# Kernel optimization log

Hardware: AMD Instinct MI355X
Metric: run time of the kernel (lower is better)

The kernel has to match this reference:

```python
import jax, jax.numpy as jnp
import numpy as np

H, QP, VP, D, DP = 4, 4, 4, 128, 64
DH = D // H


def setup_inputs() -> dict:
    key = jax.random.key(0)
    ks = jax.random.split(key, 16)
    B, L = 1, 1024
    w_c0 = float(np.log(np.e - 1.0))
    inp = {
        'single': jax.random.normal(ks[0], (B, L, D), jnp.float32),
        'pair': jax.random.normal(ks[1], (B, L, L, DP), jnp.float32),
        'T': jax.random.normal(ks[2], (B, L, 4, 4), jnp.float32),
        'w_C': jnp.full((H,), w_c0, jnp.float32),
        'ln_g': jnp.ones((D,), jnp.float32),
        'ln_b': jnp.zeros((D,), jnp.float32),
        'Wq': jax.random.normal(ks[3], (D, H * DH), jnp.float32) * 0.05,
        'Wk': jax.random.normal(ks[4], (D, H * DH), jnp.float32) * 0.05,
        'Wv': jax.random.normal(ks[5], (D, H * DH), jnp.float32) * 0.05,
        'Wqpt': jax.random.normal(ks[6], (D, H * QP * 3), jnp.float32) * 0.05,
        'Wkpt': jax.random.normal(ks[7], (D, H * QP * 3), jnp.float32) * 0.05,
        'Wvpt': jax.random.normal(ks[8], (D, H * VP * 3), jnp.float32) * 0.05,
        'Wb': jax.random.normal(ks[9], (DP, H), jnp.float32) * 0.05,
        'Wout': jax.random.normal(ks[10], (H * (DH + DP + VP * 3 + VP), D), jnp.float32) * 0.05,
        'b_out': jnp.zeros((D,), jnp.float32),
    }
    return inp


def _layernorm(x, g, b, eps=1e-5):
    x32 = x.astype(jnp.float32)
    mu = x32.mean(-1, keepdims=True)
    var = ((x32 - mu) ** 2).mean(-1, keepdims=True)
    return ((x32 - mu) * jax.lax.rsqrt(var + eps) * g + b).astype(x.dtype)


def reference(single, pair, T, w_C, ln_g, ln_b, Wq, Wk, Wv, Wqpt, Wkpt, Wvpt, Wb, Wout, b_out):
    B, L, Dm = single.shape
    scale_attn = DH ** (-0.5)
    z = _layernorm(single, ln_g, ln_b)
    Q = (z @ Wq).reshape(B, L, H, DH)
    K = (z @ Wk).reshape(B, L, H, DH)
    V = (z @ Wv).reshape(B, L, H, DH)
    Q_pt = (z @ Wqpt).reshape(B, L, H, QP, 3)
    K_pt = (z @ Wkpt).reshape(B, L, H, QP, 3)
    V_pt = (z @ Wvpt).reshape(B, L, H, VP, 3)
    R = T[..., :3, :3]   # [B,L,3,3]
    t = T[..., :3, 3]    # [B,L,3]
    # global-frame points: R @ p + t
    Q_g = jnp.einsum('blxy,blhpy->blhpx', R, Q_pt) + t[:, :, None, None, :]
    K_g = jnp.einsum('blxy,blhpy->blhpx', R, K_pt) + t[:, :, None, None, :]
    V_g = jnp.einsum('blxy,blhpy->blhpx', R, V_pt) + t[:, :, None, None, :]
    # scalar QK score [B,H,L,L]
    s_attn = jnp.einsum('bihd,bjhd->bhij', Q, K) * scale_attn
    # pair bias [B,H,L,L]
    b_attn = jnp.einsum('bijc,ch->bhij', pair, Wb)
    # squared point distance [B,H,L,L]
    diff = Q_g[:, :, None] - K_g[:, None]          # [B,L,L,H,QP,3]
    d2 = jnp.moveaxis((diff ** 2).sum((-1, -2)), -1, 1)
    w_pt = jax.nn.softplus(w_C)[None, :, None, None]
    attn = jax.nn.softmax(s_attn + b_attn - 0.5 * w_pt * d2, axis=-1)
    # scalar values [B,L,H*DH]
    o_s = jnp.einsum('bhij,bjhd->bihd', attn, V).reshape(B, L, H * DH)
    # point values aggregated in global frame then mapped back: R^T (p - t)
    o_pt_g = jnp.einsum('bhij,bjhpx->bihpx', attn, V_g)
    o_pt = jnp.einsum('blyx,blhpy->blhpx', R, o_pt_g - t[:, :, None, None, :])
    o_pt_n = jnp.sqrt((o_pt ** 2).sum(-1))
    # pair aggregation [B,L,H*DP]
    o_pair = jnp.einsum('bhij,bijc->bihc', attn, pair).reshape(B, L, H * DP)
    out = jnp.concatenate([o_s, o_pair, o_pt.reshape(B, L, -1), o_pt_n.reshape(B, L, -1)], axis=-1)
    return single + out @ Wout + b_out
```

## Files before the change

### kernel.cpp

```cpp
#include <hip/hip_runtime.h>
#include <math.h>

#define L_SEQ 1024
#define DM 128
#define JC 32
#define NCH (L_SEQ / JC)

#define OFF_KHAT 0
#define OFF_QHAT (L_SEQ * 192)
#define OFF_V    (OFF_QHAT + L_SEQ * 192)
#define OFF_VG   (OFF_V + L_SEQ * DM)

typedef __attribute__((address_space(1))) const void* gas_t;
typedef __attribute__((address_space(3))) void* las_t;

__device__ __forceinline__ void async16(const float4* g, float4* l) {
    __builtin_amdgcn_global_load_lds((gas_t)g, (las_t)l, 16, 0, 0);
}
#define ASYNC_BAR() asm volatile("s_waitcnt lgkmcnt(0)\n\ts_barrier" ::: "memory")

__global__ __launch_bounds__(256) void ipa_prep(
    const float* __restrict__ single, const float* __restrict__ T,
    const float* __restrict__ w_C, const float* __restrict__ ln_g, const float* __restrict__ ln_b,
    const float* __restrict__ Wq, const float* __restrict__ Wk, const float* __restrict__ Wv,
    const float* __restrict__ Wqpt, const float* __restrict__ Wkpt, const float* __restrict__ Wvpt,
    float* __restrict__ ws)
{
    __shared__ float z_lds[4][128];
    __shared__ float proj[4][528];
    __shared__ float qg[4][4][4][3];
    __shared__ float kg[4][4][4][3];
    __shared__ float cq[4][4], ck[4][4];

    const int t = threadIdx.x;
    const int wv = t >> 6, lane = t & 63;
    const int i0 = blockIdx.x << 2;
    const int i = i0 + wv;

    float x0 = single[i*DM + lane];
    float x1 = single[i*DM + 64 + lane];
    float s = x0 + x1, s2 = x0*x0 + x1*x1;
    #pragma unroll
    for (int off = 1; off < 64; off <<= 1) { s += __shfl_xor(s, off); s2 += __shfl_xor(s2, off); }
    float mu = s * 0.0078125f;
    float var = s2 * 0.0078125f - mu*mu;
    float rs = rsqrtf(var + 1e-5f);
    z_lds[wv][lane]      = (x0 - mu) * rs * ln_g[lane]      + ln_b[lane];
    z_lds[wv][lane + 64] = (x1 - mu) * rs * ln_g[lane + 64] + ln_b[lane + 64];
    __syncthreads();

    for (int cc = t; cc < 528; cc += 256) {
        const float* W; int col, ncol;
        if (cc < 128)      { W = Wq;   col = cc;       ncol = 128; }
        else if (cc < 256) { W = Wk;   col = cc - 128; ncol = 128; }
        else if (cc < 384) { W = Wv;   col = cc - 256; ncol = 128; }
        else if (cc < 432) { W = Wqpt; col = cc - 384; ncol = 48;  }
        else if (cc < 480) { W = Wkpt; col = cc - 432; ncol = 48;  }
        else               { W = Wvpt; col = cc - 480; ncol = 48;  }
        float a0 = 0.f, a1 = 0.f, a2 = 0.f, a3 = 0.f;
        #pragma unroll 8
        for (int k = 0; k < 128; ++k) {
            float w = W[k*ncol + col];
            a0 = fmaf(z_lds[0][k], w, a0);
            a1 = fmaf(z_lds[1][k], w, a1);
            a2 = fmaf(z_lds[2][k], w, a2);
            a3 = fmaf(z_lds[3][k], w, a3);
        }
        proj[0][cc] = a0; proj[1][cc] = a1; proj[2][cc] = a2; proj[3][cc] = a3;
    }
    __syncthreads();

    if (t < 64) {
        int r = t >> 4, h = (t >> 2) & 3, p = t & 3;
        int ii = i0 + r;
        float R[3][3], tt[3];
        #pragma unroll
        for (int x = 0; x < 3; ++x) {
            #pragma unroll
            for (int y = 0; y < 3; ++y) R[x][y] = T[ii*16 + x*4 + y];
            tt[x] = T[ii*16 + x*4 + 3];
        }
        int base = 384 + (h*4 + p)*3;
        float q0 = proj[r][base],    q1 = proj[r][base+1],  q2 = proj[r][base+2];
        float k0 = proj[r][base+48], k1 = proj[r][base+49], k2 = proj[r][base+50];
        float v0 = proj[r][base+96], v1 = proj[r][base+97], v2 = proj[r][base+98];
        #pragma unroll
        for (int x = 0; x < 3; ++x) {
            float qq = R[x][0]*q0 + R[x][1]*q1 + R[x][2]*q2 + tt[x];
            float kk = R[x][0]*k0 + R[x][1]*k1 + R[x][2]*k2 + tt[x];
            float vv = R[x][0]*v0 + R[x][1]*v1 + R[x][2]*v2 + tt[x];
            qg[r][h][p][x] = qq;
            kg[r][h][p][x] = kk;
            ws[OFF_VG + ii*48 + h*12 + p*3 + x] = vv;
        }
    }
    __syncthreads();

    if (t < 32) {
        int r = t >> 3, h = (t >> 1) & 3, isk = t & 1;
        float w = w_C[h];
        float wp = log1pf(__expf(w));
        float sq = 0.f;
        #pragma unroll
        for (int p = 0; p < 4; ++p)
            #pragma unroll
            for (int x = 0; x < 3; ++x) {
                float g = isk ? kg[r][h][p][x] : qg[r][h][p][x];
                sq += g*g;
            }
        float c = -0.5f * wp * sq;
        if (isk) ck[r][h] = c; else cq[r][h] = c;
    }
    __syncthreads();

    for (int idx = t; idx < 512; idx += 256) {
        int r = idx >> 7, d = idx & 127;
        ws[OFF_V + (size_t)(i0 + r)*DM + d] = proj[r][256 + d];
    }
    const float scale_attn = 0.17677669529663687f;
    for (int idx = t; idx < 768; idx += 256) {
        int r = idx / 192, rem = idx % 192;
        int h = rem / 48, k = rem % 48;
        int ii = i0 + r;
        float w = w_C[h];
        float wp = log1pf(__expf(w));
        float kv, qv;
        if (k < 32) {
            kv = proj[r][128 + h*32 + k];
            qv = scale_attn * proj[r][h*32 + k];
        } else if (k < 44) {
            int e = k - 32;
            kv = kg[r][h][e/3][e%3];
            qv = wp * qg[r][h][e/3][e%3];
        } else if (k == 44) { kv = ck[r][h]; qv = 1.0f; }
        else if (k == 45)   { kv = 1.0f;    qv = cq[r][h]; }
        else                { kv = 0.f;     qv = 0.f; }
        ws[OFF_KHAT + (size_t)ii*192 + h*48 + k] = kv;
        ws[OFF_QHAT + (size_t)ii*192 + h*48 + k] = qv;
    }
}

__global__ __launch_bounds__(256, 2) void ipa_attn(
    const float* __restrict__ single, const float* __restrict__ pair,
    const float* __restrict__ T, const float* __restrict__ Wb,
    const float* __restrict__ Wout, const float* __restrict__ b_out,
    const float* __restrict__ ws, float* __restrict__ out)
{
    __shared__ __align__(16) float4 pair_lds[2][2][JC][16];
    __shared__ float bias_part[4][2][JC][5];
    __shared__ float p_lds[4][2][JC];
    __shared__ float alpha_lds[4][2];
    __shared__ float l_lds[4][2];
    __shared__ __align__(16) float4 qhat_lds[2][4][12];
    __shared__ __align__(16) float4 wb_lds[64];
    __shared__ float og_lds[2][4][12];
    __shared__ __align__(16) float u_lds[2][448];

    const int t = threadIdx.x;
    const int wv = t >> 6, lane = t & 63;
    const int i0 = blockIdx.x * 2;

    if (t < 96)       ((float4*)qhat_lds)[t] = ((const float4*)(ws + OFF_QHAT))[(size_t)i0*48 + t];
    else if (t < 160) wb_lds[t - 96] = ((const float4*)Wb)[t - 96];

    const int r_b = lane >> 5, j_b = lane & 31;
    const int r_s = lane & 1,  j_s = lane >> 1;
    const int d4  = lane & 7,  jg_s = lane >> 3;
    const int c4p = lane >> 4, jg_p = lane & 15;
    const int g4  = lane & 3,  jg_g = lane >> 2;
    const int g4c = (g4 < 3) ? g4 : 0;

    float m_run = -INFINITY, l_run = 0.f;
    float4 accp[2][4];
    float4 accs[2];
    float4 accg[2];
    #pragma unroll
    for (int r = 0; r < 2; ++r) {
        accs[r] = make_float4(0.f,0.f,0.f,0.f);
        accg[r] = make_float4(0.f,0.f,0.f,0.f);
        #pragma unroll
        for (int h = 0; h < 4; ++h) accp[r][h] = make_float4(0.f,0.f,0.f,0.f);
    }

    const float4* pair4 = (const float4*)pair;
    const float4* kh4   = (const float4*)(ws + OFF_KHAT);
    const float4* v4    = (const float4*)(ws + OFF_V);
    const float4* vg4   = (const float4*)(ws + OFF_VG);
    float4* plds_flat   = &pair_lds[0][0][0][0];

    {
        #pragma unroll
        for (int it = 0; it < 4; ++it) {
            int idx = it*256 + t;
            int row = idx >> 9, j = (idx >> 4) & 31, slot = idx & 15;
            int c4 = slot ^ (j & 7);
            async16(pair4 + ((size_t)(i0 + row)*L_SEQ + j)*16 + c4, plds_flat + idx);
        }
    }

    for (int ch = 0; ch < NCH; ++ch) {
        const int cur = ch & 1;
        const int j0 = ch * JC;

        ASYNC_BAR();
        if (ch + 1 < NCH) {
            const int jn = (ch + 1) * JC;
            #pragma unroll
            for (int it = 0; it < 4; ++it) {
                int idx = it*256 + t;
                int row = idx >> 9, j = (idx >> 4) & 31, slot = idx & 15;
                int c4 = slot ^ (j & 7);
                async16(pair4 + ((size_t)(i0 + row)*L_SEQ + jn + j)*16 + c4,
                        plds_flat + (1 - cur)*1024 + idx);
            }
            asm volatile("s_waitcnt vmcnt(4)" ::: "memory");
        } else {
            asm volatile("s_waitcnt vmcnt(0)" ::: "memory");
        }
        ASYNC_BAR();

        float4 kh[12];
        {
            const float4* kp = kh4 + (size_t)(j0 + j_s)*48 + wv*12;
            #pragma unroll
            for (int k4 = 0; k4 < 12; ++k4) kh[k4] = kp[k4];
        }
        float4 vv[4];
        #pragma unroll
        for (int jj = 0; jj < 4; ++jj)
            vv[jj] = v4[(size_t)(j0 + jg_s + 8*jj)*32 + wv*8 + d4];
        float4 gvv[2];
        #pragma unroll
        for (int jj = 0; jj < 2; ++jj)
            gvv[jj] = vg4[(size_t)(j0 + jg_g + 16*jj)*12 + wv*3 + g4c];

        {
            float bx=0.f, by=0.f, bz=0.f, bw=0.f;
            #pragma unroll
            for (int cp = 0; cp < 4; ++cp) {
                int c4 = (wv << 2) + cp;
                int sw = c4 ^ (j_b & 7);
                float4 pv = pair_lds[cur][r_b][j_b][sw];
                float4 w0 = wb_lds[c4*4+0], w1 = wb_lds[c4*4+1], w2 = wb_lds[c4*4+2], w3 = wb_lds[c4*4+3];
                bx += pv.x*w0.x + pv.y*w1.x + pv.z*w2.x + pv.w*w3.x;
                by += pv.x*w0.y + pv.y*w1.y + pv.z*w2.y + pv.w*w3.y;
                bz += pv.x*w0.z + pv.y*w1.z + pv.z*w2.z + pv.w*w3.z;
                bw += pv.x*w0.w + pv.y*w1.w + pv.z*w2.w + pv.w*w3.w;
            }
            bias_part[wv][r_b][j_b][0] = bx; bias_part[wv][r_b][j_b][1] = by;
            bias_part[wv][r_b][j_b][2] = bz; bias_part[wv][r_b][j_b][3] = bw;
        }
        ASYNC_BAR();

        {
            float d = 0.f;
            #pragma unroll
            for (int k4 = 0; k4 < 12; ++k4) {
                float4 q = qhat_lds[r_s][wv][k4];
                d = fmaf(kh[k4].x, q.x, d); d = fmaf(kh[k4].y, q.y, d);
                d = fmaf(kh[k4].z, q.z, d); d = fmaf(kh[k4].w, q.w, d);
            }
            float bias = bias_part[0][r_s][j_s][wv] + bias_part[1][r_s][j_s][wv]
                       + bias_part[2][r_s][j_s][wv] + bias_part[3][r_s][j_s][wv];
            float logit = d + bias;
            float cmax = logit;
            #pragma unroll
            for (int off = 2; off < 64; off <<= 1) cmax = fmaxf(cmax, __shfl_xor(cmax, off));
            float mn = fmaxf(m_run, cmax);
            float alpha = __expf(m_run - mn);
            float p = __expf(logit - mn);
            float ps = p;
            #pragma unroll
            for (int off = 2; off < 64; off <<= 1) ps += __shfl_xor(ps, off);
            l_run = l_run * alpha + ps;
            m_run = mn;
            p_lds[wv][r_s][j_s] = p;
            if (j_s == 0) alpha_lds[wv][r_s] = alpha;
        }
        ASYNC_BAR();

        {
            float al[4][2];
            #pragma unroll
            for (int h = 0; h < 4; ++h) { al[h][0] = alpha_lds[h][0]; al[h][1] = alpha_lds[h][1]; }
            #pragma unroll
            for (int r = 0; r < 2; ++r) {
                #pragma unroll
                for (int h = 0; h < 4; ++h) {
                    float a = al[h][r];
                    accp[r][h].x *= a; accp[r][h].y *= a; accp[r][h].z *= a; accp[r][h].w *= a;
                }
                float a = al[wv][r];
                accs[r].x *= a; accs[r].y *= a; accs[r].z *= a; accs[r].w *= a;
                accg[r].x *= a; accg[r].y *= a; accg[r].z *= a; accg[r].w *= a;
            }
            #pragma unroll
            for (int jj = 0; jj < 2; ++jj) {
                int j = jg_p + 16*jj;
                int sw = ((wv << 2) + c4p) ^ (j & 7);
                #pragma unroll
                for (int r = 0; r < 2; ++r) {
                    float4 pv = pair_lds[cur][r][j][sw];
                    float p0 = p_lds[0][r][j], p1 = p_lds[1][r][j];
                    float p2 = p_lds[2][r][j], p3 = p_lds[3][r][j];
                    accp[r][0].x = fmaf(p0, pv.x, accp[r][0].x); accp[r][0].y = fmaf(p0, pv.y, accp[r][0].y);
                    accp[r][0].z = fmaf(p0, pv.z, accp[r][0].z); accp[r][0].w = fmaf(p0, pv.w, accp[r][0].w);
                    accp[r][1].x = fmaf(p1, pv.x, accp[r][1].x); accp[r][1].y = fmaf(p1, pv.y, accp[r][1].y);
                    accp[r][1].z = fmaf(p1, pv.z, accp[r][1].z); accp[r][1].w = fmaf(p1, pv.w, accp[r][1].w);
                    accp[r][2].x = fmaf(p2, pv.x, accp[r][2].x); accp[r][2].y = fmaf(p2, pv.y, accp[r][2].y);
                    accp[r][2].z = fmaf(p2, pv.z, accp[r][2].z); accp[r][2].w = fmaf(p2, pv.w, accp[r][2].w);
                    accp[r][3].x = fmaf(p3, pv.x, accp[r][3].x); accp[r][3].y = fmaf(p3, pv.y, accp[r][3].y);
                    accp[r][3].z = fmaf(p3, pv.z, accp[r][3].z); accp[r][3].w = fmaf(p3, pv.w, accp[r][3].w);
                }
            }
            #pragma unroll
            for (int jj = 0; jj < 4; ++jj) {
                int j = jg_s + 8*jj;
                float pa = p_lds[wv][0][j], pb = p_lds[wv][1][j];
                accs[0].x = fmaf(pa, vv[jj].x, accs[0].x); accs[0].y = fmaf(pa, vv[jj].y, accs[0].y);
                accs[0].z = fmaf(pa, vv[jj].z, accs[0].z); accs[0].w = fmaf(pa, vv[jj].w, accs[0].w);
                accs[1].x = fmaf(pb, vv[jj].x, accs[1].x); accs[1].y = fmaf(pb, vv[jj].y, accs[1].y);
                accs[1].z = fmaf(pb, vv[jj].z, accs[1].z); accs[1].w = fmaf(pb, vv[jj].w, accs[1].w);
            }
            #pragma unroll
            for (int jj = 0; jj < 2; ++jj) {
                int j = jg_g + 16*jj;
                float pa = p_lds[wv][0][j], pb = p_lds[wv][1][j];
                accg[0].x = fmaf(pa, gvv[jj].x, accg[0].x); accg[0].y = fmaf(pa, gvv[jj].y, accg[0].y);
                accg[0].z = fmaf(pa, gvv[jj].z, accg[0].z); accg[0].w = fmaf(pa, gvv[jj].w, accg[0].w);
                accg[1].x = fmaf(pb, gvv[jj].x, accg[1].x); accg[1].y = fmaf(pb, gvv[jj].y, accg[1].y);
                accg[1].z = fmaf(pb, gvv[jj].z, accg[1].z); accg[1].w = fmaf(pb, gvv[jj].w, accg[1].w);
            }
        }
    }

    #pragma unroll
    for (int r = 0; r < 2; ++r) {
        #pragma unroll
        for (int h = 0; h < 4; ++h) {
            #pragma unroll
            for (int off = 1; off < 16; off <<= 1) {
                accp[r][h].x += __shfl_xor(accp[r][h].x, off);
                accp[r][h].y += __shfl_xor(accp[r][h].y, off);
                accp[r][h].z += __shfl_xor(accp[r][h].z, off);
                accp[r][h].w += __shfl_xor(accp[r][h].w, off);
            }
        }
        #pragma unroll
        for (int off = 8; off < 64; off <<= 1) {
            accs[r].x += __shfl_xor(accs[r].x, off); accs[r].y += __shfl_xor(accs[r].y, off);
            accs[r].z += __shfl_xor(accs[r].z, off); accs[r].w += __shfl_xor(accs[r].w, off);
        }
        #pragma unroll
        for (int off = 4; off < 64; off <<= 1) {
            accg[r].x += __shfl_xor(accg[r].x, off); accg[r].y += __shfl_xor(accg[r].y, off);
            accg[r].z += __shfl_xor(accg[r].z, off); accg[r].w += __shfl_xor(accg[r].w, off);
        }
    }
    if (lane < 2) l_lds[wv][lane] = l_run;
    __syncthreads();
    float invl[4][2];
    #pragma unroll
    for (int h = 0; h < 4; ++h) { invl[h][0] = 1.f / l_lds[h][0]; invl[h][1] = 1.f / l_lds[h][1]; }

    if (lane < 8) {
        #pragma unroll
        for (int r = 0; r < 2; ++r) {
            float sc = invl[wv][r];
            int base = wv*32 + lane*4;
            u_lds[r][base+0] = accs[r].x*sc; u_lds[r][base+1] = accs[r].y*sc;
            u_lds[r][base+2] = accs[r].z*sc; u_lds[r][base+3] = accs[r].w*sc;
        }
    }
    if ((lane & 15) == 0) {
        int c4 = wv*4 + (lane >> 4);
        #pragma unroll
        for (int r = 0; r < 2; ++r)
            #pragma unroll
            for (int h = 0; h < 4; ++h) {
                float sc = invl[h][r];
                int base = 128 + h*64 + c4*4;
                u_lds[r][base+0] = accp[r][h].x*sc; u_lds[r][base+1] = accp[r][h].y*sc;
                u_lds[r][base+2] = accp[r][h].z*sc; u_lds[r][base+3] = accp[r][h].w*sc;
            }
    }
    if (lane < 3) {
        #pragma unroll
        for (int r = 0; r < 2; ++r) {
            float sc = invl[wv][r];
            og_lds[r][wv][lane*4+0] = accg[r].x*sc; og_lds[r][wv][lane*4+1] = accg[r].y*sc;
            og_lds[r][wv][lane*4+2] = accg[r].z*sc; og_lds[r][wv][lane*4+3] = accg[r].w*sc;
        }
    }
    __syncthreads();

    if (t < 32) {
        int r = t >> 4, idx = t & 15, h = idx >> 2, p = idx & 3;
        int ii = i0 + r;
        float R[3][3], tt[3];
        #pragma unroll
        for (int x = 0; x < 3; ++x) {
            #pragma unroll
            for (int y = 0; y < 3; ++y) R[x][y] = T[ii*16 + x*4 + y];
            tt[x] = T[ii*16 + x*4 + 3];
        }
        float v0 = og_lds[r][h][p*3+0] - tt[0];
        float v1 = og_lds[r][h][p*3+1] - tt[1];
        float v2 = og_lds[r][h][p*3+2] - tt[2];
        float n2 = 0.f;
        #pragma unroll
        for (int x = 0; x < 3; ++x) {
            float o = R[0][x]*v0 + R[1][x]*v1 + R[2][x]*v2;
            u_lds[r][384 + h*12 + p*3 + x] = o;
            n2 += o*o;
        }
        u_lds[r][432 + h*4 + p] = sqrtf(n2);
    }
    __syncthreads();

    {
        int r = t >> 7, d = t & 127;
        int ii = i0 + r;
        float acc = single[ii*DM + d] + b_out[d];
        const float4* u4 = (const float4*)u_lds[r];
        #pragma unroll 4
        for (int k4 = 0; k4 < 112; ++k4) {
            float4 u = u4[k4];
            const float* wp = Wout + (size_t)(k4*4)*128 + d;
            acc = fmaf(u.x, wp[0],   acc);
            acc = fmaf(u.y, wp[128], acc);
            acc = fmaf(u.z, wp[256], acc);
            acc = fmaf(u.w, wp[384], acc);
        }
        out[ii*DM + d] = acc;
    }
}

extern "C" void kernel_launch(void* const* d_in, const int* in_sizes, int n_in,
                              void* d_out, int out_size, void* d_ws, size_t ws_size,
                              hipStream_t stream)
{
    const float* single = (const float*)d_in[0];
    const float* pair   = (const float*)d_in[1];
    const float* T      = (const float*)d_in[2];
    const float* w_C    = (const float*)d_in[3];
    const float* ln_g   = (const float*)d_in[4];
    const float* ln_b   = (const float*)d_in[5];
    const float* Wq     = (const float*)d_in[6];
    const float* Wk     = (const float*)d_in[7];
    const float* Wv     = (const float*)d_in[8];
    const float* Wqpt   = (const float*)d_in[9];
    const float* Wkpt   = (const float*)d_in[10];
    const float* Wvpt   = (const float*)d_in[11];
    const float* Wb     = (const float*)d_in[12];
    const float* Wout   = (const float*)d_in[13];
    const float* b_out  = (const float*)d_in[14];
    float* out = (float*)d_out;
    float* ws  = (float*)d_ws;

    ipa_prep<<<256, 256, 0, stream>>>(single, T, w_C, ln_g, ln_b, Wq, Wk, Wv, Wqpt, Wkpt, Wvpt, ws);
    ipa_attn<<<512, 256, 0, stream>>>(single, pair, T, Wb, Wout, b_out, ws, out);
}
```

Measured before the change: 476.6 us.

## Process one query row per block with 64-key chunks and split output GEMV

Restructures the attention kernel so each block handles a single query row instead of two, doubling the grid to 1024 blocks. The key chunk grows from 32 to 64, so each lane owns one key and computes a whole logit per head, with no cross-lane partial sums. Launch bounds move to 4 blocks per SM, and the final Wout projection is split across both thread halves. The aim is more occupancy and parallelism, and fewer barriers per key. The cost is that K, V and Wout are now reloaded once per query row rather than once per two rows.

```diff
diff --git a/kernel.cpp b/kernel.cpp
--- a/kernel.cpp
+++ b/kernel.cpp
@@ -3,7 +3,7 @@
 
 #define L_SEQ 1024
 #define DM 128
-#define JC 32
+#define JC 64
 #define NCH (L_SEQ / JC)
 
 #define OFF_KHAT 0
@@ -140,62 +140,56 @@
     }
 }
 
-__global__ __launch_bounds__(256, 2) void ipa_attn(
+__global__ __launch_bounds__(256, 4) void ipa_attn(
     const float* __restrict__ single, const float* __restrict__ pair,
     const float* __restrict__ T, const float* __restrict__ Wb,
     const float* __restrict__ Wout, const float* __restrict__ b_out,
     const float* __restrict__ ws, float* __restrict__ out)
 {
-    __shared__ __align__(16) float4 pair_lds[2][2][JC][16];
-    __shared__ float bias_part[4][2][JC][5];
-    __shared__ float p_lds[4][2][JC];
-    __shared__ float alpha_lds[4][2];
-    __shared__ float l_lds[4][2];
-    __shared__ __align__(16) float4 qhat_lds[2][4][12];
+    __shared__ __align__(16) float4 pair_lds[2][JC][16];
+    __shared__ float bias_part[4][JC][5];
+    __shared__ __align__(16) float4 p4_lds[JC];
+    __shared__ float alpha_lds[4];
+    __shared__ float l_lds[4];
+    __shared__ __align__(16) float4 qhat_lds[4][12];
     __shared__ __align__(16) float4 wb_lds[64];
-    __shared__ float og_lds[2][4][12];
-    __shared__ __align__(16) float u_lds[2][448];
 
     const int t = threadIdx.x;
     const int wv = t >> 6, lane = t & 63;
-    const int i0 = blockIdx.x * 2;
-
-    if (t < 96)       ((float4*)qhat_lds)[t] = ((const float4*)(ws + OFF_QHAT))[(size_t)i0*48 + t];
-    else if (t < 160) wb_lds[t - 96] = ((const float4*)Wb)[t - 96];
-
-    const int r_b = lane >> 5, j_b = lane & 31;
-    const int r_s = lane & 1,  j_s = lane >> 1;
+    const int i = blockIdx.x;
+
+    if (t < 48)       ((float4*)qhat_lds)[t] = ((const float4*)(ws + OFF_QHAT))[(size_t)i*48 + t];
+    else if (t < 112) wb_lds[t - 48] = ((const float4*)Wb)[t - 48];
+
     const int d4  = lane & 7,  jg_s = lane >> 3;
     const int c4p = lane >> 4, jg_p = lane & 15;
     const int g4  = lane & 3,  jg_g = lane >> 2;
     const int g4c = (g4 < 3) ? g4 : 0;
+    const int c4o = wv << 2;
 
     float m_run = -INFINITY, l_run = 0.f;
-    float4 accp[2][4];
-    float4 accs[2];
-    float4 accg[2];
-    #pragma unroll
-    for (int r = 0; r < 2; ++r) {
-        accs[r] = make_float4(0.f,0.f,0.f,0.f);
-        accg[r] = make_float4(0.f,0.f,0.f,0.f);
-        #pragma unroll
-        for (int h = 0; h < 4; ++h) accp[r][h] = make_float4(0.f,0.f,0.f,0.f);
-    }
+    float alpha_own = 0.f;
+    float4 accp[4];
+    float4 accs;
+    float4 accg;
+    accs = make_float4(0.f,0.f,0.f,0.f);
+    accg = make_float4(0.f,0.f,0.f,0.f);
+    #pragma unroll
+    for (int h = 0; h < 4; ++h) accp[h] = make_float4(0.f,0.f,0.f,0.f);
 
     const float4* pair4 = (const float4*)pair;
     const float4* kh4   = (const float4*)(ws + OFF_KHAT);
     const float4* v4    = (const float4*)(ws + OFF_V);
     const float4* vg4   = (const float4*)(ws + OFF_VG);
-    float4* plds_flat   = &pair_lds[0][0][0][0];
-
-    {
-        #pragma unroll
-        for (int it = 0; it < 4; ++it) {
-            int idx = it*256 + t;
-            int row = idx >> 9, j = (idx >> 4) & 31, slot = idx & 15;
-            int c4 = slot ^ (j & 7);
-            async16(pair4 + ((size_t)(i0 + row)*L_SEQ + j)*16 + c4, plds_flat + idx);
-        }
+    float4* plds_flat   = &pair_lds[0][0][0];
+    float*  p_s         = (float*)p4_lds;
+
+    #pragma unroll
+    for (int it = 0; it < 4; ++it) {
+        int idx = it*256 + t;
+        int j = idx >> 4, slot = idx & 15;
+        int c4 = slot ^ (j & 7);
+        async16(pair4 + ((size_t)i*L_SEQ + j)*16 + c4, plds_flat + idx);
     }
 
     for (int ch = 0; ch < NCH; ++ch) {
@@ -208,9 +202,9 @@
             #pragma unroll
             for (int it = 0; it < 4; ++it) {
                 int idx = it*256 + t;
-                int row = idx >> 9, j = (idx >> 4) & 31, slot = idx & 15;
+                int j = idx >> 4, slot = idx & 15;
                 int c4 = slot ^ (j & 7);
-                async16(pair4 + ((size_t)(i0 + row)*L_SEQ + jn + j)*16 + c4,
+                async16(pair4 + ((size_t)i*L_SEQ + jn + j)*16 + c4,
                         plds_flat + (1 - cur)*1024 + idx);
             }
             asm volatile("s_waitcnt vmcnt(4)" ::: "memory");
@@ -221,218 +215,207 @@
 
         float4 kh[12];
         {
-            const float4* kp = kh4 + (size_t)(j0 + j_s)*48 + wv*12;
+            const float4* kp = kh4 + (size_t)(j0 + lane)*48 + wv*12;
             #pragma unroll
             for (int k4 = 0; k4 < 12; ++k4) kh[k4] = kp[k4];
         }
-        float4 vv[4];
-        #pragma unroll
-        for (int jj = 0; jj < 4; ++jj)
-            vv[jj] = v4[(size_t)(j0 + jg_s + 8*jj)*32 + wv*8 + d4];
-        float4 gvv[2];
-        #pragma unroll
-        for (int jj = 0; jj < 2; ++jj)
-            gvv[jj] = vg4[(size_t)(j0 + jg_g + 16*jj)*12 + wv*3 + g4c];
 
         {
             float bx=0.f, by=0.f, bz=0.f, bw=0.f;
             #pragma unroll
             for (int cp = 0; cp < 4; ++cp) {
-                int c4 = (wv << 2) + cp;
-                int sw = c4 ^ (j_b & 7);
-                float4 pv = pair_lds[cur][r_b][j_b][sw];
+                int c4 = c4o + cp;
+                int sw = c4 ^ (lane & 7);
+                float4 pv = pair_lds[cur][lane][sw];
                 float4 w0 = wb_lds[c4*4+0], w1 = wb_lds[c4*4+1], w2 = wb_lds[c4*4+2], w3 = wb_lds[c4*4+3];
                 bx += pv.x*w0.x + pv.y*w1.x + pv.z*w2.x + pv.w*w3.x;
                 by += pv.x*w0.y + pv.y*w1.y + pv.z*w2.y + pv.w*w3.y;
                 bz += pv.x*w0.z + pv.y*w1.z + pv.z*w2.z + pv.w*w3.z;
                 bw += pv.x*w0.w + pv.y*w1.w + pv.z*w2.w + pv.w*w3.w;
             }
-            bias_part[wv][r_b][j_b][0] = bx; bias_part[wv][r_b][j_b][1] = by;
-            bias_part[wv][r_b][j_b][2] = bz; bias_part[wv][r_b][j_b][3] = bw;
+            bias_part[wv][lane][0] = bx; bias_part[wv][lane][1] = by;
+            bias_part[wv][lane][2] = bz; bias_part[wv][lane][3] = bw;
         }
         ASYNC_BAR();
+
+        float4 vv[8];
+        float4 gvv[4];
 
         {
             float d = 0.f;
             #pragma unroll
             for (int k4 = 0; k4 < 12; ++k4) {
-                float4 q = qhat_lds[r_s][wv][k4];
+                float4 q = qhat_lds[wv][k4];
                 d = fmaf(kh[k4].x, q.x, d); d = fmaf(kh[k4].y, q.y, d);
                 d = fmaf(kh[k4].z, q.z, d); d = fmaf(kh[k4].w, q.w, d);
             }
-            float bias = bias_part[0][r_s][j_s][wv] + bias_part[1][r_s][j_s][wv]
-                       + bias_part[2][r_s][j_s][wv] + bias_part[3][r_s][j_s][wv];
+            float bias = bias_part[0][lane][wv] + bias_part[1][lane][wv]
+                       + bias_part[2][lane][wv] + bias_part[3][lane][wv];
             float logit = d + bias;
+
+            #pragma unroll
+            for (int jj = 0; jj < 8; ++jj)
+                vv[jj] = v4[(size_t)(j0 + jg_s + 8*jj)*32 + wv*8 + d4];
+            #pragma unroll
+            for (int jj = 0; jj < 4; ++jj)
+                gvv[jj] = vg4[(size_t)(j0 + jg_g + 16*jj)*12 + wv*3 + g4c];
+
             float cmax = logit;
             #pragma unroll
-            for (int off = 2; off < 64; off <<= 1) cmax = fmaxf(cmax, __shfl_xor(cmax, off));
+            for (int off = 1; off < 64; off <<= 1) cmax = fmaxf(cmax, __shfl_xor(cmax, off));
             float mn = fmaxf(m_run, cmax);
             float alpha = __expf(m_run - mn);
             float p = __expf(logit - mn);
-            float ps = p;
-            #pragma unroll
-            for (int off = 2; off < 64; off <<= 1) ps += __shfl_xor(ps, off);
-            l_run = l_run * alpha + ps;
+            l_run = l_run * alpha + p;
             m_run = mn;
-            p_lds[wv][r_s][j_s] = p;
-            if (j_s == 0) alpha_lds[wv][r_s] = alpha;
+            alpha_own = alpha;
+            p_s[lane*4 + wv] = p;
+            if (lane == 0) alpha_lds[wv] = alpha;
         }
         ASYNC_BAR();
 
         {
-            float al[4][2];
-            #pragma unroll
-            for (int h = 0; h < 4; ++h) { al[h][0] = alpha_lds[h][0]; al[h][1] = alpha_lds[h][1]; }
-            #pragma unroll
-            for (int r = 0; r < 2; ++r) {
+            float al0 = alpha_lds[0], al1 = alpha_lds[1], al2 = alpha_lds[2], al3 = alpha_lds[3];
+            accp[0].x *= al0; accp[0].y *= al0; accp[0].z *= al0; accp[0].w *= al0;
+            accp[1].x *= al1; accp[1].y *= al1; accp[1].z *= al1; accp[1].w *= al1;
+            accp[2].x *= al2; accp[2].y *= al2; accp[2].z *= al2; accp[2].w *= al2;
+            accp[3].x *= al3; accp[3].y *= al3; accp[3].z *= al3; accp[3].w *= al3;
+            accs.x *= alpha_own; accs.y *= alpha_own; accs.z *= alpha_own; accs.w *= alpha_own;
+            accg.x *= alpha_own; accg.y *= alpha_own; accg.z *= alpha_own; accg.w *= alpha_own;
+
+            {
+                int c4 = c4o + c4p;
                 #pragma unroll
-                for (int h = 0; h < 4; ++h) {
-                    float a = al[h][r];
-                    accp[r][h].x *= a; accp[r][h].y *= a; accp[r][h].z *= a; accp[r][h].w *= a;
+                for (int jj = 0; jj < 4; ++jj) {
+                    int j = jg_p + 16*jj;
+                    int sw = c4 ^ (j & 7);
+                    float4 pv = pair_lds[cur][j][sw];
+                    float4 pj = p4_lds[j];
+                    accp[0].x = fmaf(pj.x, pv.x, accp[0].x); accp[0].y = fmaf(pj.x, pv.y, accp[0].y);
+                    accp[0].z = fmaf(pj.x, pv.z, accp[0].z); accp[0].w = fmaf(pj.x, pv.w, accp[0].w);
+                    accp[1].x = fmaf(pj.y, pv.x, accp[1].x); accp[1].y = fmaf(pj.y, pv.y, accp[1].y);
+                    accp[1].z = fmaf(pj.y, pv.z, accp[1].z); accp[1].w = fmaf(pj.y, pv.w, accp[1].w);
+                    accp[2].x = fmaf(pj.z, pv.x, accp[2].x); accp[2].y = fmaf(pj.z, pv.y, accp[2].y);
+                    accp[2].z = fmaf(pj.z, pv.z, accp[2].z); accp[2].w = fmaf(pj.z, pv.w, accp[2].w);
+                    accp[3].x = fmaf(pj.w, pv.x, accp[3].x); accp[3].y = fmaf(pj.w, pv.y, accp[3].y);
+                    accp[3].z = fmaf(pj.w, pv.z, accp[3].z); accp[3].w = fmaf(pj.w, pv.w, accp[3].w);
                 }
-                float a = al[wv][r];
-                accs[r].x *= a; accs[r].y *= a; accs[r].z *= a; accs[r].w *= a;
-                accg[r].x *= a; accg[r].y *= a; accg[r].z *= a; accg[r].w *= a;
-            }
-            #pragma unroll
-            for (int jj = 0; jj < 2; ++jj) {
-                int j = jg_p + 16*jj;
-                int sw = ((wv << 2) + c4p) ^ (j & 7);
-                #pragma unroll
-                for (int r = 0; r < 2; ++r) {
-                    float4 pv = pair_lds[cur][r][j][sw];
-                    float p0 = p_lds[0][r][j], p1 = p_lds[1][r][j];
-                    float p2 = p_lds[2][r][j], p3 = p_lds[3][r][j];
-                    accp[r][0].x = fmaf(p0, pv.x, accp[r][0].x); accp[r][0].y = fmaf(p0, pv.y, accp[r][0].y);
-                    accp[r][0].z = fmaf(p0, pv.z, accp[r][0].z); accp[r][0].w = fmaf(p0, pv.w, accp[r][0].w);
-                    accp[r][1].x = fmaf(p1, pv.x, accp[r][1].x); accp[r][1].y = fmaf(p1, pv.y, accp[r][1].y);
-                    accp[r][1].z = fmaf(p1, pv.z, accp[r][1].z); accp[r][1].w = fmaf(p1, pv.w, accp[r][1].w);
-                    accp[r][2].x = fmaf(p2, pv.x, accp[r][2].x); accp[r][2].y = fmaf(p2, pv.y, accp[r][2].y);
-                    accp[r][2].z = fmaf(p2, pv.z, accp[r][2].z); accp[r][2].w = fmaf(p2, pv.w, accp[r][2].w);
-                    accp[r][3].x = fmaf(p3, pv.x, accp[r][3].x); accp[r][3].y = fmaf(p3, pv.y, accp[r][3].y);
-                    accp[r][3].z = fmaf(p3, pv.z, accp[r][3].z); accp[r][3].w = fmaf(p3, pv.w, accp[r][3].w);
-                }
+            }
+            #pragma unroll
+            for (int jj = 0; jj < 8; ++jj) {
+                int j = jg_s + 8*jj;
+                float pa = p_s[j*4 + wv];
+                accs.x = fmaf(pa, vv[jj].x, accs.x); accs.y = fmaf(pa, vv[jj].y, accs.y);
+                accs.z = fmaf(pa, vv[jj].z, accs.z); accs.w = fmaf(pa, vv[jj].w, accs.w);
             }
             #pragma unroll
             for (int jj = 0; jj < 4; ++jj) {
-                int j = jg_s + 8*jj;
-                float pa = p_lds[wv][0][j], pb = p_lds[wv][1][j];
-                accs[0].x = fmaf(pa, vv[jj].x, accs[0].x); accs[0].y = fmaf(pa, vv[jj].y, accs[0].y);
-                accs[0].z = fmaf(pa, vv[jj].z, accs[0].z); accs[0].w = fmaf(pa, vv[jj].w, accs[0].w);
-                accs[1].x = fmaf(pb, vv[jj].x, accs[1].x); accs[1].y = fmaf(pb, vv[jj].y, accs[1].y);
-                accs[1].z = fmaf(pb, vv[jj].z, accs[1].z); accs[1].w = fmaf(pb, vv[jj].w, accs[1].w);
-            }
-            #pragma unroll
-            for (int jj = 0; jj < 2; ++jj) {
                 int j = jg_g + 16*jj;
-                float pa = p_lds[wv][0][j], pb = p_lds[wv][1][j];
-                accg[0].x = fmaf(pa, gvv[jj].x, accg[0].x); accg[0].y = fmaf(pa, gvv[jj].y, accg[0].y);
-                accg[0].z = fmaf(pa, gvv[jj].z, accg[0].z); accg[0].w = fmaf(pa, gvv[jj].w, accg[0].w);
-                accg[1].x = fmaf(pb, gvv[jj].x, accg[1].x); accg[1].y = fmaf(pb, gvv[jj].y, accg[1].y);
-                accg[1].z = fmaf(pb, gvv[jj].z, accg[1].z); accg[1].w = fmaf(pb, gvv[jj].w, accg[1].w);
-            }
-        }
-    }
-
-    #pragma unroll
-    for (int r = 0; r < 2; ++r) {
+                float pa = p_s[j*4 + wv];
+                accg.x = fmaf(pa, gvv[jj].x, accg.x); accg.y = fmaf(pa, gvv[jj].y, accg.y);
+                accg.z = fmaf(pa, gvv[jj].z, accg.z); accg.w = fmaf(pa, gvv[jj].w, accg.w);
+            }
+        }
+    }
+
+    #pragma unroll
+    for (int h = 0; h < 4; ++h) {
+        #pragma unroll
+        for (int off = 1; off < 16; off <<= 1) {
+            accp[h].x += __shfl_xor(accp[h].x, off);
+            accp[h].y += __shfl_xor(accp[h].y, off);
+            accp[h].z += __shfl_xor(accp[h].z, off);
+            accp[h].w += __shfl_xor(accp[h].w, off);
+        }
+    }
+    #pragma unroll
+    for (int off = 8; off < 64; off <<= 1) {
+        accs.x += __shfl_xor(accs.x, off); accs.y += __shfl_xor(accs.y, off);
+        accs.z += __shfl_xor(accs.z, off); accs.w += __shfl_xor(accs.w, off);
+    }
+    #pragma unroll
+    for (int off = 4; off < 64; off <<= 1) {
+        accg.x += __shfl_xor(accg.x, off); accg.y += __shfl_xor(accg.y, off);
+        accg.z += __shfl_xor(accg.z, off); accg.w += __shfl_xor(accg.w, off);
+    }
+    #pragma unroll
+    for (int off = 1; off < 64; off <<= 1)
+        l_run += __shfl_xor(l_run, off);
+    if (lane == 0) l_lds[wv] = l_run;
+    __syncthreads();
+
+    float* scratch = (float*)&pair_lds[0][0][0];
+    float* u   = scratch;
+    float* og  = scratch + 448;
+    float* tmp = scratch + 512;
+
+    float invl[4];
+    #pragma unroll
+    for (int h = 0; h < 4; ++h) invl[h] = 1.f / l_lds[h];
+
+    if (lane < 8) {
+        float sc = invl[wv];
+        int base = wv*32 + lane*4;
+        u[base+0] = accs.x*sc; u[base+1] = accs.y*sc;
+        u[base+2] = accs.z*sc; u[base+3] = accs.w*sc;
+    }
+    if ((lane & 15) == 0) {
+        int c4 = c4o + (lane >> 4);
         #pragma unroll
         for (int h = 0; h < 4; ++h) {
-            #pragma unroll
-            for (int off = 1; off < 16; off <<= 1) {
-                accp[r][h].x += __shfl_xor(accp[r][h].x, off);
-                accp[r][h].y += __shfl_xor(accp[r][h].y, off);
-                accp[r][h].z += __shfl_xor(accp[r][h].z, off);
-                accp[r][h].w += __shfl_xor(accp[r][h].w, off);
-            }
-        }
-        #pragma unroll
-        for (int off = 8; off < 64; off <<= 1) {
-            accs[r].x += __shfl_xor(accs[r].x, off); accs[r].y += __shfl_xor(accs[r].y, off);
-            accs[r].z += __shfl_xor(accs[r].z, off); accs[r].w += __shfl_xor(accs[r].w, off);
-        }
-        #pragma unroll
-        for (int off = 4; off < 64; off <<= 1) {
-            accg[r].x += __shfl_xor(accg[r].x, off); accg[r].y += __shfl_xor(accg[r].y, off);
-            accg[r].z += __shfl_xor(accg[r].z, off); accg[r].w += __shfl_xor(accg[r].w, off);
-        }
-    }
-    if (lane < 2) l_lds[wv][lane] = l_run;
-    __syncthreads();
-    float invl[4][2];
-    #pragma unroll
-    for (int h = 0; h < 4; ++h) { invl[h][0] = 1.f / l_lds[h][0]; invl[h][1] = 1.f / l_lds[h][1]; }
-
-    if (lane < 8) {
-        #pragma unroll
-        for (int r = 0; r < 2; ++r) {
-            float sc = invl[wv][r];
-            int base = wv*32 + lane*4;
-            u_lds[r][base+0] = accs[r].x*sc; u_lds[r][base+1] = accs[r].y*sc;
-            u_lds[r][base+2] = accs[r].z*sc; u_lds[r][base+3] = accs[r].w*sc;
-        }
-    }
-    if ((lane & 15) == 0) {
-        int c4 = wv*4 + (lane >> 4);
-        #pragma unroll
-        for (int r = 0; r < 2; ++r)
-            #pragma unroll
-            for (int h = 0; h < 4; ++h) {
-                float sc = invl[h][r];
-                int base = 128 + h*64 + c4*4;
-                u_lds[r][base+0] = accp[r][h].x*sc; u_lds[r][base+1] = accp[r][h].y*sc;
-                u_lds[r][base+2] = accp[r][h].z*sc; u_lds[r][base+3] = accp[r][h].w*sc;
-            }
+            float sc = invl[h];
+            int base = 128 + h*64 + c4*4;
+            u[base+0] = accp[h].x*sc; u[base+1] = accp[h].y*sc;
+            u[base+2] = accp[h].z*sc; u[base+3] = accp[h].w*sc;
+        }
     }
     if (lane < 3) {
-        #pragma unroll
-        for (int r = 0; r < 2; ++r) {
-            float sc = invl[wv][r];
-            og_lds[r][wv][lane*4+0] = accg[r].x*sc; og_lds[r][wv][lane*4+1] = accg[r].y*sc;
-            og_lds[r][wv][lane*4+2] = accg[r].z*sc; og_lds[r][wv][lane*4+3] = accg[r].w*sc;
-        }
-    }
-    __syncthreads();
-
-    if (t < 32) {
-        int r = t >> 4, idx = t & 15, h = idx >> 2, p = idx & 3;
-        int ii = i0 + r;
+        float sc = invl[wv];
+        og[wv*12 + lane*4+0] = accg.x*sc; og[wv*12 + lane*4+1] = accg.y*sc;
+        og[wv*12 + lane*4+2] = accg.z*sc; og[wv*12 + lane*4+3] = accg.w*sc;
+    }
+    __syncthreads();
+
+    if (t < 16) {
+        int h = t >> 2, p = t & 3;
         float R[3][3], tt[3];
         #pragma unroll
         for (int x = 0; x < 3; ++x) {
             #pragma unroll
-            for (int y = 0; y < 3; ++y) R[x][y] = T[ii*16 + x*4 + y];
-            tt[x] = T[ii*16 + x*4 + 3];
-        }
-        float v0 = og_lds[r][h][p*3+0] - tt[0];
-        float v1 = og_lds[r][h][p*3+1] - tt[1];
-        float v2 = og_lds[r][h][p*3+2] - tt[2];
+            for (int y = 0; y < 3; ++y) R[x][y] = T[i*16 + x*4 + y];
+            tt[x] = T[i*16 + x*4 + 3];
+        }
+        float v0 = og[h*12 + p*3+0] - tt[0];
+        float v1 = og[h*12 + p*3+1] - tt[1];
+        float v2 = og[h*12 + p*3+2] - tt[2];
         float n2 = 0.f;
         #pragma unroll
         for (int x = 0; x < 3; ++x) {
             float o = R[0][x]*v0 + R[1][x]*v1 + R[2][x]*v2;
-            u_lds[r][384 + h*12 + p*3 + x] = o;
+            u[384 + h*12 + p*3 + x] = o;
             n2 += o*o;
         }
-        u_lds[r][432 + h*4 + p] = sqrtf(n2);
+        u[432 + h*4 + p] = sqrtf(n2);
     }
     __syncthreads();
 
     {
-        int r = t >> 7, d = t & 127;
-        int ii = i0 + r;
-        float acc = single[ii*DM + d] + b_out[d];
-        const float4* u4 = (const float4*)u_lds[r];
+        int d = t & 127, khalf = t >> 7;
+        float acc = 0.f;
+        const float4* u4 = (const float4*)u;
+        int k0 = khalf * 56;
         #pragma unroll 4
-        for (int k4 = 0; k4 < 112; ++k4) {
-            float4 u = u4[k4];
+        for (int k4 = k0; k4 < k0 + 56; ++k4) {
+            float4 uu = u4[k4];
             const float* wp = Wout + (size_t)(k4*4)*128 + d;
-            acc = fmaf(u.x, wp[0],   acc);
-            acc = fmaf(u.y, wp[128], acc);
-            acc = fmaf(u.z, wp[256], acc);
-            acc = fmaf(u.w, wp[384], acc);
-        }
-        out[ii*DM + d] = acc;
+            acc = fmaf(uu.x, wp[0],   acc);
+            acc = fmaf(uu.y, wp[128], acc);
+            acc = fmaf(uu.z, wp[256], acc);
+            acc = fmaf(uu.w, wp[384], acc);
+        }
+        if (khalf) tmp[d] = acc;
+        __syncthreads();
+        if (!khalf) out[i*DM + d] = single[i*DM + d] + b_out[d] + acc + tmp[d];
     }
 }
 
@@ -459,5 +442,5 @@
     float* ws  = (float*)d_ws;
 
     ipa_prep<<<256, 256, 0, stream>>>(single, T, w_C, ln_g, ln_b, Wq, Wk, Wv, Wqpt, Wkpt, Wvpt, ws);
-    ipa_attn<<<512, 256, 0, stream>>>(single, pair, T, Wb, Wout, b_out, ws, out);
+    ipa_attn<<<1024, 256, 0, stream>>>(single, pair, T, Wb, Wout, b_out, ws, out);
 }
```

After: 626.2 us. 1.31x slower.
